# Kernel tuning notes

Measured on AMD Instinct MI355X. Metric: run time of the kernel, lower is better.

## Reference

```python
import jax, jax.numpy as jnp
import numpy as np

# ---- constants from the adaptive-LIF (ALIF) cell in the efficient_spiking_networks repo ----
B_J0 = 0.01     # baseline threshold
BETA = 1.8      # adaptation coupling
LENS = 0.5      # surrogate-gradient width
SCALE = 6.0
HIGHT = 0.15
GAMMA = 0.5

B, C, T, D = 512, 3, 500, 40
N, OUT = 256, 12


@jax.custom_vjp
def spike_fn(x):
    return (x > 0.0).astype(x.dtype)

def _spike_fwd(x):
    return spike_fn(x), x

def _spike_bwd(x, g):
    def gauss(v, mu, sigma):
        return jnp.exp(-((v - mu) ** 2) / (2.0 * sigma * sigma)) / (jnp.sqrt(2.0 * jnp.pi) * sigma)
    sur = GAMMA * (gauss(x, 0.0, LENS) * (1.0 + HIGHT)
                   - gauss(x, LENS, SCALE * LENS) * HIGHT
                   - gauss(x, -LENS, SCALE * LENS) * HIGHT)
    return (g * sur,)

spike_fn.defvjp(_spike_fwd, _spike_bwd)


def setup_inputs() -> dict:
    key = jax.random.key(0)
    ks = jax.random.split(key, 16)
    xav1 = float(np.sqrt(2.0 / (C * D + N)))
    xav3 = float(np.sqrt(2.0 / (N + OUT)))
    kai = float(np.sqrt(2.0 / N))
    return {
        'x': jax.random.normal(ks[0], (B, C, T, D), dtype=jnp.float32),
        'thr': jnp.array(0.05, dtype=jnp.float32),
        'W1': jax.random.normal(ks[1], (N, C * D), dtype=jnp.float32) * xav1,
        'b1': jnp.zeros((N,), dtype=jnp.float32),
        'W2_in': jax.random.normal(ks[2], (N, N), dtype=jnp.float32) * float(np.sqrt(1.0 / N)),
        'b2_in': jnp.zeros((N,), dtype=jnp.float32),
        'W2_rec': jax.random.normal(ks[3], (N, N), dtype=jnp.float32) * kai,
        'b2_rec': jnp.zeros((N,), dtype=jnp.float32),
        'W3': jax.random.normal(ks[4], (OUT, N), dtype=jnp.float32) * xav3,
        'b3': jnp.zeros((OUT,), dtype=jnp.float32),
        'tau_adp1': 200.0 + 50.0 * jax.random.normal(ks[5], (N,), dtype=jnp.float32),
        'tau_m1': 20.0 + 5.0 * jax.random.normal(ks[6], (N,), dtype=jnp.float32),
        'tau_adp2': 200.0 + 50.0 * jax.random.normal(ks[7], (N,), dtype=jnp.float32),
        'tau_m2': 20.0 + 5.0 * jax.random.normal(ks[8], (N,), dtype=jnp.float32),
        'tau_m3': 10.0 + 1.0 * jax.random.normal(ks[9], (OUT,), dtype=jnp.float32),
    }


def _alif(I, mem, spk, badp, alpha, rho):
    # adaptive threshold update with previous spike, then LIF membrane update
    badp = rho * badp + (1.0 - rho) * spk
    Bth = B_J0 + BETA * badp
    mem = alpha * mem + (1.0 - alpha) * I - Bth * spk
    s = spike_fn(mem - Bth)
    return mem, s, badp


def reference(x, thr, W1, b1, W2_in, b2_in, W2_rec, b2_rec, W3, b3,
              tau_adp1, tau_m1, tau_adp2, tau_m2, tau_m3):
    b, c, t, d = x.shape
    # ternary input spikification through surrogate step
    xs = spike_fn(x - thr) - spike_fn(-thr - x)          # [b,c,t,d] in {-1,0,1}
    xs = jnp.transpose(xs, (2, 0, 1, 3)).reshape(t, b, c * d)  # [t,b,c*d]

    alpha1 = jnp.exp(-1.0 / tau_m1)
    rho1 = jnp.exp(-1.0 / tau_adp1)
    alpha2 = jnp.exp(-1.0 / tau_m2)
    rho2 = jnp.exp(-1.0 / tau_adp2)
    alpha3 = jnp.exp(-1.0 / tau_m3)

    n = W1.shape[0]
    out = W3.shape[0]
    z = lambda m: jnp.zeros((b, m), dtype=x.dtype)
    carry0 = (z(n), z(n), jnp.full((b, n), B_J0, x.dtype),
              z(n), z(n), jnp.full((b, n), B_J0, x.dtype),
              z(out), z(out))

    def step(carry, x_t):
        m1, s1, a1, m2, s2, a2, m3, acc = carry
        i1 = x_t @ W1.T + b1
        m1, s1, a1 = _alif(i1, m1, s1, a1, alpha1, rho1)
        i2 = s1 @ W2_in.T + b2_in + s2 @ W2_rec.T + b2_rec
        m2, s2, a2 = _alif(i2, m2, s2, a2, alpha2, rho2)
        i3 = s2 @ W3.T + b3
        m3 = alpha3 * m3 + (1.0 - alpha3) * i3
        acc = acc + m3
        return (m1, s1, a1, m2, s2, a2, m3, acc), None

    carry, _ = jax.lax.scan(step, carry0, xs)
    acc = carry[-1]
    return jax.nn.log_softmax(acc / t, axis=1)
```

## Files before the change

### kernel.cpp

```cpp
#include <hip/hip_runtime.h>
#include <math.h>

#define B_   512
#define C_   3
#define T_   500
#define D_   40
#define CD_  120
#define N_   256
#define OUT_ 12
#define TILE 8
#define NTILE 63

#define W1T_OFF  0
#define W2IT_OFF 30720
#define W2RT_OFF (30720 + 65792)

__global__ void prep_kernel(const float* __restrict__ W1, const float* __restrict__ W2i,
                            const float* __restrict__ W2r, float* __restrict__ ws) {
    int i = blockIdx.x * 256 + threadIdx.x;
    int k = i >> 8, n = i & 255;
    if (k < 256) {
        ws[W2IT_OFF + i] = W2i[n * 256 + k];
        ws[W2RT_OFF + i] = W2r[n * 256 + k];
    } else if (k == 256) {
        ws[W2IT_OFF + i] = 0.f;
        ws[W2RT_OFF + i] = 0.f;
    }
    if (i < CD_ * N_) ws[W1T_OFF + i] = W1[n * CD_ + k];
}

__device__ __forceinline__ void alif_step(float I, float& m, float& s, float& a,
                                          float al, float rh) {
    a = rh * a + (1.f - rh) * s;
    float Bth = 0.01f + 1.8f * a;
    m = al * m + (1.f - al) * I - Bth * s;
    s = ((m - Bth) > 0.f) ? 1.f : 0.f;
}

__device__ __forceinline__ void gather16(const float* __restrict__ Wt,
                                         const int* __restrict__ L,
                                         const float2* __restrict__ M,
                                         int cnt, int n, float& g0, float& g1) {
    int j = 0;
    for (; j + 16 <= cnt; j += 16) {
        int4 ia = *(const int4*)(L + j);
        int4 ib = *(const int4*)(L + j + 4);
        int4 ic = *(const int4*)(L + j + 8);
        int4 id = *(const int4*)(L + j + 12);
        float4 ma = *(const float4*)(M + j);
        float4 mb = *(const float4*)(M + j + 2);
        float4 mc = *(const float4*)(M + j + 4);
        float4 md = *(const float4*)(M + j + 6);
        float4 me = *(const float4*)(M + j + 8);
        float4 mf = *(const float4*)(M + j + 10);
        float4 mg = *(const float4*)(M + j + 12);
        float4 mh = *(const float4*)(M + j + 14);
        float w0  = Wt[(ia.x << 8) + n];
        float w1  = Wt[(ia.y << 8) + n];
        float w2  = Wt[(ia.z << 8) + n];
        float w3  = Wt[(ia.w << 8) + n];
        float w4  = Wt[(ib.x << 8) + n];
        float w5  = Wt[(ib.y << 8) + n];
        float w6  = Wt[(ib.z << 8) + n];
        float w7  = Wt[(ib.w << 8) + n];
        float w8  = Wt[(ic.x << 8) + n];
        float w9  = Wt[(ic.y << 8) + n];
        float w10 = Wt[(ic.z << 8) + n];
        float w11 = Wt[(ic.w << 8) + n];
        float w12 = Wt[(id.x << 8) + n];
        float w13 = Wt[(id.y << 8) + n];
        float w14 = Wt[(id.z << 8) + n];
        float w15 = Wt[(id.w << 8) + n];
        g0 += w0*ma.x;  g1 += w0*ma.y;  g0 += w1*ma.z;  g1 += w1*ma.w;
        g0 += w2*mb.x;  g1 += w2*mb.y;  g0 += w3*mb.z;  g1 += w3*mb.w;
        g0 += w4*mc.x;  g1 += w4*mc.y;  g0 += w5*mc.z;  g1 += w5*mc.w;
        g0 += w6*md.x;  g1 += w6*md.y;  g0 += w7*md.z;  g1 += w7*md.w;
        g0 += w8*me.x;  g1 += w8*me.y;  g0 += w9*me.z;  g1 += w9*me.w;
        g0 += w10*mf.x; g1 += w10*mf.y; g0 += w11*mf.z; g1 += w11*mf.w;
        g0 += w12*mg.x; g1 += w12*mg.y; g0 += w13*mg.z; g1 += w13*mg.w;
        g0 += w14*mh.x; g1 += w14*mh.y; g0 += w15*mh.z; g1 += w15*mh.w;
    }
    if (j < cnt) {
        int4 ia = *(const int4*)(L + j);
        int4 ib = *(const int4*)(L + j + 4);
        float4 ma = *(const float4*)(M + j);
        float4 mb = *(const float4*)(M + j + 2);
        float4 mc = *(const float4*)(M + j + 4);
        float4 md = *(const float4*)(M + j + 6);
        float w0 = Wt[(ia.x << 8) + n];
        float w1 = Wt[(ia.y << 8) + n];
        float w2 = Wt[(ia.z << 8) + n];
        float w3 = Wt[(ia.w << 8) + n];
        float w4 = Wt[(ib.x << 8) + n];
        float w5 = Wt[(ib.y << 8) + n];
        float w6 = Wt[(ib.z << 8) + n];
        float w7 = Wt[(ib.w << 8) + n];
        g0 += w0*ma.x; g1 += w0*ma.y; g0 += w1*ma.z; g1 += w1*ma.w;
        g0 += w2*mb.x; g1 += w2*mb.y; g0 += w3*mb.z; g1 += w3*mb.w;
        g0 += w4*mc.x; g1 += w4*mc.y; g0 += w5*mc.z; g1 += w5*mc.w;
        g0 += w6*md.x; g1 += w6*md.y; g0 += w7*md.z; g1 += w7*md.w;
    }
}

__global__ __launch_bounds__(512, 2) void scan_kernel(
    const float* __restrict__ x, const float* __restrict__ thr_p,
    const float* __restrict__ b1, const float* __restrict__ b2i,
    const float* __restrict__ b2r, const float* __restrict__ b3,
    const float* __restrict__ tau_adp1, const float* __restrict__ tau_m1,
    const float* __restrict__ tau_adp2, const float* __restrict__ tau_m2,
    const float* __restrict__ tau_m3, const float* __restrict__ W3,
    const float* __restrict__ ws, float* __restrict__ out) {

    __shared__ float xsf_t[2][TILE][CD_];
    __shared__ __align__(16) float xsf8[2][CD_][TILE];
    __shared__ __align__(16) int    idx1[2][4][72];
    __shared__ __align__(16) int    idx2[2][4][72];
    __shared__ __align__(16) float2 mf1[2][4][72];
    __shared__ __align__(16) float2 mf2[2][4][72];
    __shared__ int cw1[2][4], cw2[2][4];
    __shared__ float part[2][2][N_];
    __shared__ float red[2][OUT_][4];
    __shared__ float accs_l[2][OUT_];

    const int tid  = threadIdx.x;
    const int n    = tid & 255;
    const int h    = tid >> 8;
    const int wv   = tid >> 6;
    const int seg  = wv & 3;
    const int lane = tid & 63;
    const int b0   = blockIdx.x * 2;

    const float* W1T  = ws + W1T_OFF;
    const float* W2iT = ws + W2IT_OFF;
    const float* W2rT = ws + W2RT_OFF;

    const float thrv = thr_p[0];
    const float al1 = expf(-1.0f / tau_m1[n]);
    const float rh1 = expf(-1.0f / tau_adp1[n]);
    const float al2 = expf(-1.0f / tau_m2[n]);
    const float rh2 = expf(-1.0f / tau_adp2[n]);
    const float b1v = b1[n];
    const float b2v = b2i[n] + b2r[n];

    float al3j[OUT_];
    #pragma unroll
    for (int o = 0; o < OUT_; ++o) al3j[o] = expf(-1.0f / tau_m3[o]);

    float m1[2] = {0.f, 0.f}, s1f[2] = {0.f, 0.f}, a1v[2] = {0.01f, 0.01f};
    float m2[2] = {0.f, 0.f}, s2f[2] = {0.f, 0.f}, a2v[2] = {0.01f, 0.01f};
    float S[2] = {0.f, 0.f};
    float P[2][OUT_];
    #pragma unroll
    for (int g = 0; g < 2; ++g)
        #pragma unroll
        for (int o = 0; o < OUT_; ++o) P[g][o] = 0.f;

    if (tid < 4) cw2[1][tid] = 0;
    const unsigned long long lmask = (1ull << lane) - 1ull;

    float xreg[4];
    #pragma unroll
    for (int j = 0; j < 4; ++j) {
        int idx = tid + j * 512;
        if (idx < 2 * TILE * CD_) {
            int g = idx / (TILE * CD_), r = idx % (TILE * CD_);
            int tt = r / CD_, k = r % CD_;
            int c = k / D_, d = k - c * D_;
            int tg = tt; if (tg > T_ - 1) tg = T_ - 1;
            xreg[j] = x[((b0 + g) * C_ + c) * (T_ * D_) + tg * D_ + d];
        }
    }

    #pragma unroll 1
    for (int it = 0; it < NTILE; ++it) {
        const int t0 = it * TILE;

        #pragma unroll
        for (int j = 0; j < 4; ++j) {
            int idx = tid + j * 512;
            if (idx < 2 * TILE * CD_) {
                int g = idx / (TILE * CD_), r = idx % (TILE * CD_);
                int tt = r / CD_, k = r % CD_;
                float xv = xreg[j];
                float tp = ((xv - thrv)  > 0.f) ? 1.f : 0.f;
                float tn = ((-thrv - xv) > 0.f) ? 1.f : 0.f;
                xsf_t[g][tt][k] = tp - tn;
            }
        }
        __syncthreads();

        if (it + 1 < NTILE) {
            const int t0n = (it + 1) * TILE;
            #pragma unroll
            for (int j = 0; j < 4; ++j) {
                int idx = tid + j * 512;
                if (idx < 2 * TILE * CD_) {
                    int g = idx / (TILE * CD_), r = idx % (TILE * CD_);
                    int tt = r / CD_, k = r % CD_;
                    int c = k / D_, d = k - c * D_;
                    int tg = t0n + tt; if (tg > T_ - 1) tg = T_ - 1;
                    xreg[j] = x[((b0 + g) * C_ + c) * (T_ * D_) + tg * D_ + d];
                }
            }
        }

        #pragma unroll
        for (int j = 0; j < 4; ++j) {
            int idx = tid + j * 512;
            if (idx < 2 * TILE * CD_) {
                int g = idx / (TILE * CD_), r = idx % (TILE * CD_);
                int k = r / TILE, tt = r % TILE;
                xsf8[g][k][tt] = xsf_t[g][tt][k];
            }
        }
        __syncthreads();

        float i1a[2][TILE];
        #pragma unroll
        for (int g = 0; g < 2; ++g)
            #pragma unroll
            for (int tt = 0; tt < TILE; ++tt) i1a[g][tt] = 0.f;
        {
            const float* wc = W1T + n;
            #pragma unroll 4
            for (int k = 0; k < CD_; ++k) {
                float w = wc[k << 8];
                float4 xa0 = *(const float4*)&xsf8[0][k][0];
                float4 xa1 = *(const float4*)&xsf8[0][k][4];
                float4 xb0 = *(const float4*)&xsf8[1][k][0];
                float4 xb1 = *(const float4*)&xsf8[1][k][4];
                i1a[0][0] += xa0.x * w; i1a[0][1] += xa0.y * w;
                i1a[0][2] += xa0.z * w; i1a[0][3] += xa0.w * w;
                i1a[0][4] += xa1.x * w; i1a[0][5] += xa1.y * w;
                i1a[0][6] += xa1.z * w; i1a[0][7] += xa1.w * w;
                i1a[1][0] += xb0.x * w; i1a[1][1] += xb0.y * w;
                i1a[1][2] += xb0.z * w; i1a[1][3] += xb0.w * w;
                i1a[1][4] += xb1.x * w; i1a[1][5] += xb1.y * w;
                i1a[1][6] += xb1.z * w; i1a[1][7] += xb1.w * w;
            }
        }

        #pragma unroll
        for (int tt = 0; tt < TILE; ++tt) {
            const int t = t0 + tt;
            const int pp = t & 1, pq = pp ^ 1;

            alif_step(b1v + i1a[0][tt], m1[0], s1f[0], a1v[0], al1, rh1);
            alif_step(b1v + i1a[1][tt], m1[1], s1f[1], a1v[1], al1, rh1);

            {
                bool p0 = s1f[0] > 0.5f, p1 = s1f[1] > 0.5f;
                unsigned long long bu = __ballot(p0) | __ballot(p1);
                if (h == 0) {
                    int cnt = __popcll(bu), cpad = (cnt + 7) & ~7;
                    if (p0 | p1) {
                        int r = __popcll(bu & lmask);
                        idx1[pp][seg][r] = n;
                        mf1[pp][seg][r] = make_float2(p0 ? 1.f : 0.f, p1 ? 1.f : 0.f);
                    } else {
                        int nr = __popcll(~bu & lmask);
                        if (nr < cpad - cnt) {
                            idx1[pp][seg][cnt + nr] = 256;
                            mf1[pp][seg][cnt + nr] = make_float2(0.f, 0.f);
                        }
                    }
                    if (lane == 0) cw1[pp][seg] = cpad;
                }
            }
            __syncthreads();

            float g0 = 0.f, g1 = 0.f;
            {
                int sa = 2 * h, sb = 2 * h + 1;
                gather16(W2iT, &idx1[pp][sa][0], &mf1[pp][sa][0], cw1[pp][sa], n, g0, g1);
                gather16(W2iT, &idx1[pp][sb][0], &mf1[pp][sb][0], cw1[pp][sb], n, g0, g1);
                gather16(W2rT, &idx2[pq][sa][0], &mf2[pq][sa][0], cw2[pq][sa], n, g0, g1);
                gather16(W2rT, &idx2[pq][sb][0], &mf2[pq][sb][0], cw2[pq][sb], n, g0, g1);
            }
            part[h][0][n] = g0;
            part[h][1][n] = g1;
            __syncthreads();

            float i20 = b2v + part[0][0][n] + part[1][0][n];
            float i21 = b2v + part[0][1][n] + part[1][1][n];
            alif_step(i20, m2[0], s2f[0], a2v[0], al2, rh2);
            alif_step(i21, m2[1], s2f[1], a2v[1], al2, rh2);

            {
                bool p0 = s2f[0] > 0.5f, p1 = s2f[1] > 0.5f;
                unsigned long long bu = __ballot(p0) | __ballot(p1);
                if (h == 1) {
                    int cnt = __popcll(bu), cpad = (cnt + 7) & ~7;
                    if (p0 | p1) {
                        int r = __popcll(bu & lmask);
                        idx2[pp][seg][r] = n;
                        mf2[pp][seg][r] = make_float2(p0 ? 1.f : 0.f, p1 ? 1.f : 0.f);
                    } else {
                        int nr = __popcll(~bu & lmask);
                        if (nr < cpad - cnt) {
                            idx2[pp][seg][cnt + nr] = 256;
                            mf2[pp][seg][cnt + nr] = make_float2(0.f, 0.f);
                        }
                    }
                    if (lane == 0) cw2[pp][seg] = cpad;
                }
            }

            if (t < T_) {
                #pragma unroll
                for (int g = 0; g < 2; ++g) {
                    S[g] += s2f[g];
                    #pragma unroll
                    for (int o = 0; o < OUT_; ++o)
                        P[g][o] = al3j[o] * (P[g][o] + s2f[g]);
                }
            }
        }
    }

    if (h == 0) {
        #pragma unroll
        for (int g = 0; g < 2; ++g) {
            #pragma unroll
            for (int o = 0; o < OUT_; ++o) {
                float v = W3[o * N_ + n] * (S[g] - P[g][o]);
                v += __shfl_down(v, 32);
                v += __shfl_down(v, 16);
                v += __shfl_down(v, 8);
                v += __shfl_down(v, 4);
                v += __shfl_down(v, 2);
                v += __shfl_down(v, 1);
                if (lane == 0) red[g][o][seg] = v;
            }
        }
    }
    __syncthreads();
    if (tid < 24) {
        int g = tid / OUT_, o = tid % OUT_;
        float acc = red[g][o][0] + red[g][o][1] + red[g][o][2] + red[g][o][3];
        float al3 = al3j[o];
        float alT = expf(-(float)T_ / tau_m3[o]);
        float Co  = (float)T_ - al3 * (1.f - alT) / (1.f - al3);
        acc += b3[o] * Co;
        accs_l[g][o] = acc / (float)T_;
    }
    __syncthreads();
    if (tid < 24) {
        int g = tid / OUT_, o = tid % OUT_;
        float mx = -1e30f;
        #pragma unroll
        for (int o2 = 0; o2 < OUT_; ++o2) mx = fmaxf(mx, accs_l[g][o2]);
        float se = 0.f;
        #pragma unroll
        for (int o2 = 0; o2 < OUT_; ++o2) se += expf(accs_l[g][o2] - mx);
        out[(b0 + g) * OUT_ + o] = accs_l[g][o] - mx - logf(se);
    }
}

extern "C" void kernel_launch(void* const* d_in, const int* in_sizes, int n_in,
                              void* d_out, int out_size, void* d_ws, size_t ws_size,
                              hipStream_t stream) {
    (void)in_sizes; (void)n_in; (void)out_size; (void)ws_size;
    const float* x        = (const float*)d_in[0];
    const float* thr      = (const float*)d_in[1];
    const float* W1       = (const float*)d_in[2];
    const float* b1       = (const float*)d_in[3];
    const float* W2_in    = (const float*)d_in[4];
    const float* b2_in    = (const float*)d_in[5];
    const float* W2_rec   = (const float*)d_in[6];
    const float* b2_rec   = (const float*)d_in[7];
    const float* W3       = (const float*)d_in[8];
    const float* b3       = (const float*)d_in[9];
    const float* tau_adp1 = (const float*)d_in[10];
    const float* tau_m1   = (const float*)d_in[11];
    const float* tau_adp2 = (const float*)d_in[12];
    const float* tau_m2   = (const float*)d_in[13];
    const float* tau_m3   = (const float*)d_in[14];
    float* ws  = (float*)d_ws;
    float* out = (float*)d_out;

    prep_kernel<<<257, 256, 0, stream>>>(W1, W2_in, W2_rec, ws);
    scan_kernel<<<B_ / 2, 512, 0, stream>>>(x, thr, b1, b2_in, b2_rec, b3,
                                            tau_adp1, tau_m1, tau_adp2, tau_m2,
                                            tau_m3, W3, ws, out);
}
```

Before: 1.809 ms.

## Store recurrent weights in fp16 and split scan work over 1024 threads

Recurrent weight matrices are converted to half precision in the prep kernel, which halves the bytes gathered per spike. The scan kernel moves from 512 to 1024 threads per block: the layer-1 input projection is split over four thread groups and written to shared memory, and the sparse spike gathers are split over four quarter-groups whose partial sums are reduced in shared memory. Layer-1 and layer-2 ALIF updates now run on separate halves of the block, with an extra barrier per tile. The changes risk lower occupancy (one block per CU), more synchronisation, and precision loss in the recurrent weights.

```diff
diff --git a/kernel.cpp b/kernel.cpp
--- a/kernel.cpp
+++ b/kernel.cpp
@@ -1,4 +1,5 @@
 #include <hip/hip_runtime.h>
+#include <hip/hip_fp16.h>
 #include <math.h>
 
 #define B_   512
@@ -11,22 +12,23 @@
 #define TILE 8
 #define NTILE 63
 
-#define W1T_OFF  0
-#define W2IT_OFF 30720
-#define W2RT_OFF (30720 + 65792)
+#define W1T_F    30720
+#define W2I_H_OFF 0
+#define W2R_H_OFF 65792
 
 __global__ void prep_kernel(const float* __restrict__ W1, const float* __restrict__ W2i,
                             const float* __restrict__ W2r, float* __restrict__ ws) {
+    __half* wsh = (__half*)(ws + W1T_F);
     int i = blockIdx.x * 256 + threadIdx.x;
     int k = i >> 8, n = i & 255;
     if (k < 256) {
-        ws[W2IT_OFF + i] = W2i[n * 256 + k];
-        ws[W2RT_OFF + i] = W2r[n * 256 + k];
+        wsh[W2I_H_OFF + i] = __float2half(W2i[n * 256 + k]);
+        wsh[W2R_H_OFF + i] = __float2half(W2r[n * 256 + k]);
     } else if (k == 256) {
-        ws[W2IT_OFF + i] = 0.f;
-        ws[W2RT_OFF + i] = 0.f;
-    }
-    if (i < CD_ * N_) ws[W1T_OFF + i] = W1[n * CD_ + k];
+        wsh[W2I_H_OFF + i] = __float2half(0.f);
+        wsh[W2R_H_OFF + i] = __float2half(0.f);
+    }
+    if (i < CD_ * N_) ws[i] = W1[n * CD_ + k];
 }
 
 __device__ __forceinline__ void alif_step(float I, float& m, float& s, float& a,
@@ -37,10 +39,10 @@
     s = ((m - Bth) > 0.f) ? 1.f : 0.f;
 }
 
-__device__ __forceinline__ void gather16(const float* __restrict__ Wt,
-                                         const int* __restrict__ L,
-                                         const float2* __restrict__ M,
-                                         int cnt, int n, float& g0, float& g1) {
+__device__ __forceinline__ void gather16h(const __half* __restrict__ Wt,
+                                          const int* __restrict__ L,
+                                          const float2* __restrict__ M,
+                                          int cnt, int n, float& g0, float& g1) {
     int j = 0;
     for (; j + 16 <= cnt; j += 16) {
         int4 ia = *(const int4*)(L + j);
@@ -55,22 +57,22 @@
         float4 mf = *(const float4*)(M + j + 10);
         float4 mg = *(const float4*)(M + j + 12);
         float4 mh = *(const float4*)(M + j + 14);
-        float w0  = Wt[(ia.x << 8) + n];
-        float w1  = Wt[(ia.y << 8) + n];
-        float w2  = Wt[(ia.z << 8) + n];
-        float w3  = Wt[(ia.w << 8) + n];
-        float w4  = Wt[(ib.x << 8) + n];
-        float w5  = Wt[(ib.y << 8) + n];
-        float w6  = Wt[(ib.z << 8) + n];
-        float w7  = Wt[(ib.w << 8) + n];
-        float w8  = Wt[(ic.x << 8) + n];
-        float w9  = Wt[(ic.y << 8) + n];
-        float w10 = Wt[(ic.z << 8) + n];
-        float w11 = Wt[(ic.w << 8) + n];
-        float w12 = Wt[(id.x << 8) + n];
-        float w13 = Wt[(id.y << 8) + n];
-        float w14 = Wt[(id.z << 8) + n];
-        float w15 = Wt[(id.w << 8) + n];
+        float w0  = __half2float(Wt[(ia.x << 8) + n]);
+        float w1  = __half2float(Wt[(ia.y << 8) + n]);
+        float w2  = __half2float(Wt[(ia.z << 8) + n]);
+        float w3  = __half2float(Wt[(ia.w << 8) + n]);
+        float w4  = __half2float(Wt[(ib.x << 8) + n]);
+        float w5  = __half2float(Wt[(ib.y << 8) + n]);
+        float w6  = __half2float(Wt[(ib.z << 8) + n]);
+        float w7  = __half2float(Wt[(ib.w << 8) + n]);
+        float w8  = __half2float(Wt[(ic.x << 8) + n]);
+        float w9  = __half2float(Wt[(ic.y << 8) + n]);
+        float w10 = __half2float(Wt[(ic.z << 8) + n]);
+        float w11 = __half2float(Wt[(ic.w << 8) + n]);
+        float w12 = __half2float(Wt[(id.x << 8) + n]);
+        float w13 = __half2float(Wt[(id.y << 8) + n]);
+        float w14 = __half2float(Wt[(id.z << 8) + n]);
+        float w15 = __half2float(Wt[(id.w << 8) + n]);
         g0 += w0*ma.x;  g1 += w0*ma.y;  g0 += w1*ma.z;  g1 += w1*ma.w;
         g0 += w2*mb.x;  g1 += w2*mb.y;  g0 += w3*mb.z;  g1 += w3*mb.w;
         g0 += w4*mc.x;  g1 += w4*mc.y;  g0 += w5*mc.z;  g1 += w5*mc.w;
@@ -87,14 +89,14 @@
         float4 mb = *(const float4*)(M + j + 2);
         float4 mc = *(const float4*)(M + j + 4);
         float4 md = *(const float4*)(M + j + 6);
-        float w0 = Wt[(ia.x << 8) + n];
-        float w1 = Wt[(ia.y << 8) + n];
-        float w2 = Wt[(ia.z << 8) + n];
-        float w3 = Wt[(ia.w << 8) + n];
-        float w4 = Wt[(ib.x << 8) + n];
-        float w5 = Wt[(ib.y << 8) + n];
-        float w6 = Wt[(ib.z << 8) + n];
-        float w7 = Wt[(ib.w << 8) + n];
+        float w0 = __half2float(Wt[(ia.x << 8) + n]);
+        float w1 = __half2float(Wt[(ia.y << 8) + n]);
+        float w2 = __half2float(Wt[(ia.z << 8) + n]);
+        float w3 = __half2float(Wt[(ia.w << 8) + n]);
+        float w4 = __half2float(Wt[(ib.x << 8) + n]);
+        float w5 = __half2float(Wt[(ib.y << 8) + n]);
+        float w6 = __half2float(Wt[(ib.z << 8) + n]);
+        float w7 = __half2float(Wt[(ib.w << 8) + n]);
         g0 += w0*ma.x; g1 += w0*ma.y; g0 += w1*ma.z; g1 += w1*ma.w;
         g0 += w2*mb.x; g1 += w2*mb.y; g0 += w3*mb.z; g1 += w3*mb.w;
         g0 += w4*mc.x; g1 += w4*mc.y; g0 += w5*mc.z; g1 += w5*mc.w;
@@ -102,7 +104,7 @@
     }
 }
 
-__global__ __launch_bounds__(512, 2) void scan_kernel(
+__global__ __launch_bounds__(1024, 1) void scan_kernel(
     const float* __restrict__ x, const float* __restrict__ thr_p,
     const float* __restrict__ b1, const float* __restrict__ b2i,
     const float* __restrict__ b2r, const float* __restrict__ b3,
@@ -113,26 +115,27 @@
 
     __shared__ float xsf_t[2][TILE][CD_];
     __shared__ __align__(16) float xsf8[2][CD_][TILE];
+    __shared__ float i1s[2][TILE][N_];
     __shared__ __align__(16) int    idx1[2][4][72];
     __shared__ __align__(16) int    idx2[2][4][72];
     __shared__ __align__(16) float2 mf1[2][4][72];
     __shared__ __align__(16) float2 mf2[2][4][72];
     __shared__ int cw1[2][4], cw2[2][4];
-    __shared__ float part[2][2][N_];
+    __shared__ float part[4][2][N_];
     __shared__ float red[2][OUT_][4];
     __shared__ float accs_l[2][OUT_];
 
     const int tid  = threadIdx.x;
     const int n    = tid & 255;
     const int h    = tid >> 8;
-    const int wv   = tid >> 6;
-    const int seg  = wv & 3;
+    const int seg  = (tid >> 6) & 3;
     const int lane = tid & 63;
     const int b0   = blockIdx.x * 2;
 
-    const float* W1T  = ws + W1T_OFF;
-    const float* W2iT = ws + W2IT_OFF;
-    const float* W2rT = ws + W2RT_OFF;
+    const float* W1T = ws;
+    const __half* wsh  = (const __half*)(ws + W1T_F);
+    const __half* W2iH = wsh + W2I_H_OFF;
+    const __half* W2rH = wsh + W2R_H_OFF;
 
     const float thrv = thr_p[0];
     const float al1 = expf(-1.0f / tau_m1[n]);
@@ -158,10 +161,12 @@
     if (tid < 4) cw2[1][tid] = 0;
     const unsigned long long lmask = (1ull << lane) - 1ull;
 
-    float xreg[4];
+    const int gq = h & 1, tb = h >> 1;
+
+    float xreg[2];
     #pragma unroll
-    for (int j = 0; j < 4; ++j) {
-        int idx = tid + j * 512;
+    for (int j = 0; j < 2; ++j) {
+        int idx = tid + j * 1024;
         if (idx < 2 * TILE * CD_) {
             int g = idx / (TILE * CD_), r = idx % (TILE * CD_);
             int tt = r / CD_, k = r % CD_;
@@ -176,8 +181,8 @@
         const int t0 = it * TILE;
 
         #pragma unroll
-        for (int j = 0; j < 4; ++j) {
-            int idx = tid + j * 512;
+        for (int j = 0; j < 2; ++j) {
+            int idx = tid + j * 1024;
             if (idx < 2 * TILE * CD_) {
                 int g = idx / (TILE * CD_), r = idx % (TILE * CD_);
                 int tt = r / CD_, k = r % CD_;
@@ -192,8 +197,8 @@
         if (it + 1 < NTILE) {
             const int t0n = (it + 1) * TILE;
             #pragma unroll
-            for (int j = 0; j < 4; ++j) {
-                int idx = tid + j * 512;
+            for (int j = 0; j < 2; ++j) {
+                int idx = tid + j * 1024;
                 if (idx < 2 * TILE * CD_) {
                     int g = idx / (TILE * CD_), r = idx % (TILE * CD_);
                     int tt = r / CD_, k = r % CD_;
@@ -205,8 +210,8 @@
         }
 
         #pragma unroll
-        for (int j = 0; j < 4; ++j) {
-            int idx = tid + j * 512;
+        for (int j = 0; j < 2; ++j) {
+            int idx = tid + j * 1024;
             if (idx < 2 * TILE * CD_) {
                 int g = idx / (TILE * CD_), r = idx % (TILE * CD_);
                 int k = r / TILE, tt = r % TILE;
@@ -215,110 +220,92 @@
         }
         __syncthreads();
 
-        float i1a[2][TILE];
-        #pragma unroll
-        for (int g = 0; g < 2; ++g)
-            #pragma unroll
-            for (int tt = 0; tt < TILE; ++tt) i1a[g][tt] = 0.f;
         {
+            float acc0 = 0.f, acc1 = 0.f, acc2 = 0.f, acc3 = 0.f;
             const float* wc = W1T + n;
             #pragma unroll 4
             for (int k = 0; k < CD_; ++k) {
                 float w = wc[k << 8];
-                float4 xa0 = *(const float4*)&xsf8[0][k][0];
-                float4 xa1 = *(const float4*)&xsf8[0][k][4];
-                float4 xb0 = *(const float4*)&xsf8[1][k][0];
-                float4 xb1 = *(const float4*)&xsf8[1][k][4];
-                i1a[0][0] += xa0.x * w; i1a[0][1] += xa0.y * w;
-                i1a[0][2] += xa0.z * w; i1a[0][3] += xa0.w * w;
-                i1a[0][4] += xa1.x * w; i1a[0][5] += xa1.y * w;
-                i1a[0][6] += xa1.z * w; i1a[0][7] += xa1.w * w;
-                i1a[1][0] += xb0.x * w; i1a[1][1] += xb0.y * w;
-                i1a[1][2] += xb0.z * w; i1a[1][3] += xb0.w * w;
-                i1a[1][4] += xb1.x * w; i1a[1][5] += xb1.y * w;
-                i1a[1][6] += xb1.z * w; i1a[1][7] += xb1.w * w;
-            }
-        }
+                float4 xa = *(const float4*)&xsf8[gq][k][tb * 4];
+                acc0 += xa.x * w; acc1 += xa.y * w;
+                acc2 += xa.z * w; acc3 += xa.w * w;
+            }
+            i1s[gq][tb * 4 + 0][n] = acc0;
+            i1s[gq][tb * 4 + 1][n] = acc1;
+            i1s[gq][tb * 4 + 2][n] = acc2;
+            i1s[gq][tb * 4 + 3][n] = acc3;
+        }
+        __syncthreads();
 
         #pragma unroll
         for (int tt = 0; tt < TILE; ++tt) {
             const int t = t0 + tt;
             const int pp = t & 1, pq = pp ^ 1;
 
-            alif_step(b1v + i1a[0][tt], m1[0], s1f[0], a1v[0], al1, rh1);
-            alif_step(b1v + i1a[1][tt], m1[1], s1f[1], a1v[1], al1, rh1);
-
-            {
+            if (h == 0) {
+                alif_step(b1v + i1s[0][tt][n], m1[0], s1f[0], a1v[0], al1, rh1);
+                alif_step(b1v + i1s[1][tt][n], m1[1], s1f[1], a1v[1], al1, rh1);
                 bool p0 = s1f[0] > 0.5f, p1 = s1f[1] > 0.5f;
                 unsigned long long bu = __ballot(p0) | __ballot(p1);
-                if (h == 0) {
-                    int cnt = __popcll(bu), cpad = (cnt + 7) & ~7;
-                    if (p0 | p1) {
-                        int r = __popcll(bu & lmask);
-                        idx1[pp][seg][r] = n;
-                        mf1[pp][seg][r] = make_float2(p0 ? 1.f : 0.f, p1 ? 1.f : 0.f);
-                    } else {
-                        int nr = __popcll(~bu & lmask);
-                        if (nr < cpad - cnt) {
-                            idx1[pp][seg][cnt + nr] = 256;
-                            mf1[pp][seg][cnt + nr] = make_float2(0.f, 0.f);
-                        }
+                int cnt = __popcll(bu), cpad = (cnt + 7) & ~7;
+                if (p0 | p1) {
+                    int r = __popcll(bu & lmask);
+                    idx1[pp][seg][r] = n;
+                    mf1[pp][seg][r] = make_float2(p0 ? 1.f : 0.f, p1 ? 1.f : 0.f);
+                } else {
+                    int nr = __popcll(~bu & lmask);
+                    if (nr < cpad - cnt) {
+                        idx1[pp][seg][cnt + nr] = 256;
+                        mf1[pp][seg][cnt + nr] = make_float2(0.f, 0.f);
                     }
-                    if (lane == 0) cw1[pp][seg] = cpad;
                 }
+                if (lane == 0) cw1[pp][seg] = cpad;
             }
             __syncthreads();
 
             float g0 = 0.f, g1 = 0.f;
-            {
-                int sa = 2 * h, sb = 2 * h + 1;
-                gather16(W2iT, &idx1[pp][sa][0], &mf1[pp][sa][0], cw1[pp][sa], n, g0, g1);
-                gather16(W2iT, &idx1[pp][sb][0], &mf1[pp][sb][0], cw1[pp][sb], n, g0, g1);
-                gather16(W2rT, &idx2[pq][sa][0], &mf2[pq][sa][0], cw2[pq][sa], n, g0, g1);
-                gather16(W2rT, &idx2[pq][sb][0], &mf2[pq][sb][0], cw2[pq][sb], n, g0, g1);
-            }
+            gather16h(W2iH, &idx1[pp][h][0], &mf1[pp][h][0], cw1[pp][h], n, g0, g1);
+            gather16h(W2rH, &idx2[pq][h][0], &mf2[pq][h][0], cw2[pq][h], n, g0, g1);
             part[h][0][n] = g0;
             part[h][1][n] = g1;
             __syncthreads();
 
-            float i20 = b2v + part[0][0][n] + part[1][0][n];
-            float i21 = b2v + part[0][1][n] + part[1][1][n];
-            alif_step(i20, m2[0], s2f[0], a2v[0], al2, rh2);
-            alif_step(i21, m2[1], s2f[1], a2v[1], al2, rh2);
-
-            {
+            if (h == 1) {
+                float i20 = b2v + ((part[0][0][n] + part[1][0][n]) +
+                                   (part[2][0][n] + part[3][0][n]));
+                float i21 = b2v + ((part[0][1][n] + part[1][1][n]) +
+                                   (part[2][1][n] + part[3][1][n]));
+                alif_step(i20, m2[0], s2f[0], a2v[0], al2, rh2);
+                alif_step(i21, m2[1], s2f[1], a2v[1], al2, rh2);
                 bool p0 = s2f[0] > 0.5f, p1 = s2f[1] > 0.5f;
                 unsigned long long bu = __ballot(p0) | __ballot(p1);
-                if (h == 1) {
-                    int cnt = __popcll(bu), cpad = (cnt + 7) & ~7;
-                    if (p0 | p1) {
-                        int r = __popcll(bu & lmask);
-                        idx2[pp][seg][r] = n;
-                        mf2[pp][seg][r] = make_float2(p0 ? 1.f : 0.f, p1 ? 1.f : 0.f);
-                    } else {
-                        int nr = __popcll(~bu & lmask);
-                        if (nr < cpad - cnt) {
-                            idx2[pp][seg][cnt + nr] = 256;
-                            mf2[pp][seg][cnt + nr] = make_float2(0.f, 0.f);
-                        }
+                int cnt = __popcll(bu), cpad = (cnt + 7) & ~7;
+                if (p0 | p1) {
+                    int r = __popcll(bu & lmask);
+                    idx2[pp][seg][r] = n;
+                    mf2[pp][seg][r] = make_float2(p0 ? 1.f : 0.f, p1 ? 1.f : 0.f);
+                } else {
+                    int nr = __popcll(~bu & lmask);
+                    if (nr < cpad - cnt) {
+                        idx2[pp][seg][cnt + nr] = 256;
+                        mf2[pp][seg][cnt + nr] = make_float2(0.f, 0.f);
                     }
-                    if (lane == 0) cw2[pp][seg] = cpad;
                 }
-            }
-
-            if (t < T_) {
-                #pragma unroll
-                for (int g = 0; g < 2; ++g) {
-                    S[g] += s2f[g];
+                if (lane == 0) cw2[pp][seg] = cpad;
+                if (t < T_) {
+                    S[0] += s2f[0]; S[1] += s2f[1];
                     #pragma unroll
-                    for (int o = 0; o < OUT_; ++o)
-                        P[g][o] = al3j[o] * (P[g][o] + s2f[g]);
+                    for (int o = 0; o < OUT_; ++o) {
+                        P[0][o] = al3j[o] * (P[0][o] + s2f[0]);
+                        P[1][o] = al3j[o] * (P[1][o] + s2f[1]);
+                    }
                 }
             }
         }
-    }
-
-    if (h == 0) {
+        __syncthreads();
+    }
+
+    if (h == 1) {
         #pragma unroll
         for (int g = 0; g < 2; ++g) {
             #pragma unroll
@@ -380,7 +367,7 @@
     float* out = (float*)d_out;
 
     prep_kernel<<<257, 256, 0, stream>>>(W1, W2_in, W2_rec, ws);
-    scan_kernel<<<B_ / 2, 512, 0, stream>>>(x, thr, b1, b2_in, b2_rec, b3,
-                                            tau_adp1, tau_m1, tau_adp2, tau_m2,
-                                            tau_m3, W3, ws, out);
-}
+    scan_kernel<<<B_ / 2, 1024, 0, stream>>>(x, thr, b1, b2_in, b2_rec, b3,
+                                             tau_adp1, tau_m1, tau_adp2, tau_m2,
+                                             tau_m3, W3, ws, out);
+}
```

Result: slower. 2.452 ms (+35.6%).
